# Kernel tuning notes

Measured on AMD Instinct MI355X. Metric: run time of the kernel, lower is better.

The kernel has to match this reference:

```python
import jax, jax.numpy as jnp
import numpy as np

DIV_COEF = 1.0
EPS = 1e-8  # torch.cosine_similarity default eps


def setup_inputs() -> dict:
    key = jax.random.key(0)
    id_ = jax.random.normal(key, (8192, 512), dtype=jnp.float32)
    return {"id": id_}


def reference(id):
    # cosine similarity via norm + GEMM (math identical to broadcast form)
    norms = jnp.linalg.norm(id, axis=1)                      # [N]
    dots = id @ id.T                                          # [N, N]
    sim = dots / jnp.maximum(norms[:, None] * norms[None, :], EPS)
    n = id.shape[0]
    # zero diagonal, clamp negatives to zero, mean over full NxN
    off_diag = 1.0 - jnp.eye(n, dtype=sim.dtype)
    id_sim = off_diag * sim
    l_id_div = jnp.mean(jnp.where(id_sim < 0, 0.0, id_sim))
    total_loss = DIV_COEF * l_id_div
    return (total_loss, l_id_div)
```

## Files before the change

### kernel.cpp

```cpp
#include <hip/hip_runtime.h>
#include <stdint.h>

#define NROWS 8192
#define KDIM  512
#define BM    128
#define BK    128
#define NKI   (KDIM / BK)
#define NT    (NROWS / BM)
#define NBLK  (NT * (NT + 1) / 2)

typedef __attribute__((ext_vector_type(4)))  int   i32x4;
typedef __attribute__((ext_vector_type(8)))  int   i32x8;
typedef __attribute__((ext_vector_type(16))) float f32x16;

#define SCALE1 0x7F7F7F7Fu

__device__ __forceinline__ void async_copy16(const unsigned char* g, unsigned char* l) {
  __builtin_amdgcn_global_load_lds(
      (const __attribute__((address_space(1))) unsigned int*)g,
      (__attribute__((address_space(3))) unsigned int*)l,
      16, 0, 0);
}

__global__ __launch_bounds__(256) void prep_kernel(
    const float* __restrict__ src, unsigned char* __restrict__ dst,
    float* __restrict__ acc) {
  const int row  = blockIdx.x * 4 + (threadIdx.x >> 6);
  const int lane = threadIdx.x & 63;
  const float4 v0 = ((const float4*)src)[row * 128 + lane * 2];
  const float4 v1 = ((const float4*)src)[row * 128 + lane * 2 + 1];
  float ss = v0.x * v0.x + v0.y * v0.y + v0.z * v0.z + v0.w * v0.w
           + v1.x * v1.x + v1.y * v1.y + v1.z * v1.z + v1.w * v1.w;
  #pragma unroll
  for (int off = 32; off > 0; off >>= 1) ss += __shfl_down(ss, off);
  const float rn = 1.0f / sqrtf(__shfl(ss, 0));
  if (row == 0 && lane == 0) *acc = 0.0f;
  int pk0 = __builtin_amdgcn_cvt_pk_fp8_f32(v0.x * rn, v0.y * rn, 0, false);
  pk0     = __builtin_amdgcn_cvt_pk_fp8_f32(v0.z * rn, v0.w * rn, pk0, true);
  int pk1 = __builtin_amdgcn_cvt_pk_fp8_f32(v1.x * rn, v1.y * rn, 0, false);
  pk1     = __builtin_amdgcn_cvt_pk_fp8_f32(v1.z * rn, v1.w * rn, pk1, true);
  const int cg  = lane >> 1;
  const int win = cg >> 3;
  const int p   = (cg & 7) ^ (row & 7);
  uint2 o; o.x = (unsigned int)pk0; o.y = (unsigned int)pk1;
  ((uint2*)dst)[row * 64 + win * 16 + p * 2 + (lane & 1)] = o;
}

__device__ __forceinline__ int tri_base(int b) {
  return b * NT - (b * (b - 1)) / 2;
}

__global__ __launch_bounds__(256) void sim_reduce_kernel(
    const unsigned char* __restrict__ idn, float* __restrict__ acc) {
  const int idx = blockIdx.x;
  const float Af = 2.0f * NT + 1.0f;
  int bi = (int)((Af - sqrtf(Af * Af - 8.0f * (float)idx)) * 0.5f);
  while (bi > 0 && tri_base(bi) > idx) bi--;
  while (tri_base(bi + 1) <= idx) bi++;
  const int bj = bi + (idx - tri_base(bi));

  __shared__ __align__(16) unsigned char As[2][BM * BK];
  __shared__ __align__(16) unsigned char Bs[2][BM * BK];

  const int tid  = threadIdx.x;
  const int lane = tid & 63;
  const int w    = tid >> 6;
  const int wr   = (w >> 1) * 64;
  const int wc   = (w & 1) * 64;
  const int l31  = lane & 31;
  const int kg   = lane >> 5;
  const int key  = lane & 7;

  f32x16 acc_f[2][2];
  #pragma unroll
  for (int i = 0; i < 2; i++)
    #pragma unroll
    for (int j = 0; j < 2; j++)
      #pragma unroll
      for (int k = 0; k < 16; k++) acc_f[i][j][k] = 0.f;

  const unsigned char* gA = idn + (size_t)(bi * BM + (tid >> 3)) * KDIM + (tid & 7) * 16;
  const unsigned char* gB = idn + (size_t)(bj * BM + (tid >> 3)) * KDIM + (tid & 7) * 16;
  const int ldso = tid * 16;

  #pragma unroll
  for (int i = 0; i < 4; i++) async_copy16(gA + (size_t)i * 16384, &As[0][ldso + i * 4096]);
  #pragma unroll
  for (int i = 0; i < 4; i++) async_copy16(gB + (size_t)i * 16384, &Bs[0][ldso + i * 4096]);

  #pragma unroll
  for (int t = 0; t < NKI; ++t) {
    const int cs = t & 1;
    if (t + 1 < NKI) {
      const int ns = cs ^ 1;
      const int ko = (t + 1) * BK;
      #pragma unroll
      for (int i = 0; i < 4; i++)
        async_copy16(gA + ko + (size_t)i * 16384, &As[ns][ldso + i * 4096]);
      #pragma unroll
      for (int i = 0; i < 4; i++)
        async_copy16(gB + ko + (size_t)i * 16384, &Bs[ns][ldso + i * 4096]);
      asm volatile("s_waitcnt vmcnt(8)" ::: "memory");
    } else {
      asm volatile("s_waitcnt vmcnt(0)" ::: "memory");
    }
    asm volatile("s_barrier" ::: "memory");

    #pragma unroll
    for (int s = 0; s < 2; s++) {
      const int c0 = s * 4 + kg * 2;
      const int pA0 = (c0 ^ key) * 16, pA1 = ((c0 + 1) ^ key) * 16;
      i32x8 a[2], b[2];
      #pragma unroll
      for (int r = 0; r < 2; r++) {
        const int rowA = (wr + r * 32 + l31) * BK;
        const int rowB = (wc + r * 32 + l31) * BK;
        i32x4 alo = *(const i32x4*)&As[cs][rowA + pA0];
        i32x4 ahi = *(const i32x4*)&As[cs][rowA + pA1];
        i32x4 blo = *(const i32x4*)&Bs[cs][rowB + pA0];
        i32x4 bhi = *(const i32x4*)&Bs[cs][rowB + pA1];
        a[r] = __builtin_shufflevector(alo, ahi, 0, 1, 2, 3, 4, 5, 6, 7);
        b[r] = __builtin_shufflevector(blo, bhi, 0, 1, 2, 3, 4, 5, 6, 7);
      }
      #pragma unroll
      for (int r = 0; r < 2; r++)
        #pragma unroll
        for (int c = 0; c < 2; c++)
          acc_f[r][c] = __builtin_amdgcn_mfma_scale_f32_32x32x64_f8f6f4(
              a[r], b[c], acc_f[r][c], 0, 0,
              0, SCALE1, 0, SCALE1);
    }

    asm volatile("s_barrier" ::: "memory");
  }

  float local = 0.f;
  const bool diag = (bi == bj);
  #pragma unroll
  for (int r = 0; r < 2; r++)
    #pragma unroll
    for (int c = 0; c < 2; c++)
      #pragma unroll
      for (int k = 0; k < 16; k++) {
        const int ri = wr + r * 32 + (k & 3) + 8 * (k >> 2) + 4 * kg;
        const int ci = wc + c * 32 + l31;
        float v = fmaxf(acc_f[r][c][k], 0.f);
        if (diag && ri == ci) v = 0.f;
        local += v;
      }

  #pragma unroll
  for (int off = 32; off > 0; off >>= 1) local += __shfl_down(local, off);
  __syncthreads();
  float* red = (float*)As;
  if (lane == 0) red[w] = local;
  __syncthreads();
  if (tid == 0) {
    float s = red[0] + red[1] + red[2] + red[3];
    if (!diag) s *= 2.f;
    atomicAdd(acc, s);
  }
}

__global__ void finalize_kernel(const float* __restrict__ acc, float* __restrict__ out) {
  const float m = *acc * (1.0f / ((float)NROWS * (float)NROWS));
  out[0] = m;
  out[1] = m;
}

extern "C" void kernel_launch(void* const* d_in, const int* in_sizes, int n_in,
                              void* d_out, int out_size, void* d_ws, size_t ws_size,
                              hipStream_t stream) {
  const float* id = (const float*)d_in[0];
  float* out = (float*)d_out;
  unsigned char* idn = (unsigned char*)d_ws;
  float* acc = (float*)((char*)d_ws + (size_t)NROWS * KDIM);

  prep_kernel<<<NROWS / 4, 256, 0, stream>>>(id, idn, acc);
  sim_reduce_kernel<<<NBLK, 256, 0, stream>>>(idn, acc);
  finalize_kernel<<<1, 1, 0, stream>>>(acc, out);
}
```

Baseline: 98.75 us.

## Keep A row-panel in registers and stream several B tiles per block

Each block now loads its full 128x512 FP8 A panel once into registers (via LDS) and loops over up to four B column tiles. B tiles are streamed in two K-halves through double-buffered LDS stages. This amortizes the A loads and cuts the block count, which should reduce global traffic, launch overhead and the triangular-index math. The cost is much higher register pressure (launch bounds with 2 blocks/CU), 64KB of LDS per block, and wasted blocks that exit early in the upper grid region.

```diff
diff --git a/kernel.cpp b/kernel.cpp
--- a/kernel.cpp
+++ b/kernel.cpp
@@ -3,11 +3,9 @@
 
 #define NROWS 8192
 #define KDIM  512
-#define BM    128
-#define BK    128
-#define NKI   (KDIM / BK)
-#define NT    (NROWS / BM)
-#define NBLK  (NT * (NT + 1) / 2)
+#define SR    128
+#define NT    (NROWS / SR)
+#define JCH   4
 
 typedef __attribute__((ext_vector_type(4)))  int   i32x4;
 typedef __attribute__((ext_vector_type(8)))  int   i32x8;
@@ -46,21 +44,17 @@
   ((uint2*)dst)[row * 64 + win * 16 + p * 2 + (lane & 1)] = o;
 }
 
-__device__ __forceinline__ int tri_base(int b) {
-  return b * NT - (b * (b - 1)) / 2;
-}
+__global__ __launch_bounds__(256, 2) void sim_reduce_kernel(
+    const unsigned char* __restrict__ idn, float* __restrict__ acc) {
+  const int bi = blockIdx.y;
+  const int jc = blockIdx.x;
+  if (jc * JCH + JCH <= bi) return;
+  const int j0 = (bi > jc * JCH) ? bi : jc * JCH;
+  const int j1 = jc * JCH + JCH;
 
-__global__ __launch_bounds__(256) void sim_reduce_kernel(
-    const unsigned char* __restrict__ idn, float* __restrict__ acc) {
-  const int idx = blockIdx.x;
-  const float Af = 2.0f * NT + 1.0f;
-  int bi = (int)((Af - sqrtf(Af * Af - 8.0f * (float)idx)) * 0.5f);
-  while (bi > 0 && tri_base(bi) > idx) bi--;
-  while (tri_base(bi + 1) <= idx) bi++;
-  const int bj = bi + (idx - tri_base(bi));
-
-  __shared__ __align__(16) unsigned char As[2][BM * BK];
-  __shared__ __align__(16) unsigned char Bs[2][BM * BK];
+  __shared__ __align__(16) unsigned char smem[65536];
+  unsigned char* st0 = smem;
+  unsigned char* st1 = smem + 32768;
 
   const int tid  = threadIdx.x;
   const int lane = tid & 63;
@@ -69,97 +63,113 @@
   const int wc   = (w & 1) * 64;
   const int l31  = lane & 31;
   const int kg   = lane >> 5;
-  const int key  = lane & 7;
 
-  f32x16 acc_f[2][2];
+  {
+    const unsigned char* gA = idn + (size_t)(bi * SR + (tid >> 5)) * KDIM + (tid & 31) * 16;
+    #pragma unroll
+    for (int i = 0; i < 16; i++)
+      async_copy16(gA + (size_t)i * 8 * KDIM, smem + tid * 16 + i * 4096);
+    asm volatile("s_waitcnt vmcnt(0)" ::: "memory");
+    __syncthreads();
+  }
+  i32x8 af[2][8];
+  #pragma unroll
+  for (int rt = 0; rt < 2; rt++) {
+    const int row = wr + rt * 32 + l31;
+    const int r7  = row & 7;
+    #pragma unroll
+    for (int s = 0; s < 8; s++) {
+      const int c0 = s * 4 + kg * 2;
+      const int ad = row * 512 + (c0 >> 3) * 128 + ((c0 & 7) ^ r7) * 16;
+      i32x4 lo = *(const i32x4*)&smem[ad];
+      i32x4 hi = *(const i32x4*)&smem[ad ^ 16];
+      af[rt][s] = __builtin_shufflevector(lo, hi, 0, 1, 2, 3, 4, 5, 6, 7);
+    }
+  }
+  asm volatile("s_waitcnt lgkmcnt(0)" ::: "memory");
+  __syncthreads();
+
+  f32x16 accf[2][2];
   #pragma unroll
   for (int i = 0; i < 2; i++)
     #pragma unroll
     for (int j = 0; j < 2; j++)
       #pragma unroll
-      for (int k = 0; k < 16; k++) acc_f[i][j][k] = 0.f;
+      for (int k = 0; k < 16; k++) accf[i][j][k] = 0.f;
+  float local = 0.f;
 
-  const unsigned char* gA = idn + (size_t)(bi * BM + (tid >> 3)) * KDIM + (tid & 7) * 16;
-  const unsigned char* gB = idn + (size_t)(bj * BM + (tid >> 3)) * KDIM + (tid & 7) * 16;
-  const int ldso = tid * 16;
-
-  #pragma unroll
-  for (int i = 0; i < 4; i++) async_copy16(gA + (size_t)i * 16384, &As[0][ldso + i * 4096]);
-  #pragma unroll
-  for (int i = 0; i < 4; i++) async_copy16(gB + (size_t)i * 16384, &Bs[0][ldso + i * 4096]);
-
-  #pragma unroll
-  for (int t = 0; t < NKI; ++t) {
-    const int cs = t & 1;
-    if (t + 1 < NKI) {
-      const int ns = cs ^ 1;
-      const int ko = (t + 1) * BK;
+  auto fillB = [&](int jj, int kh, unsigned char* stg) {
+    const unsigned char* gB =
+        idn + (size_t)(jj * SR + (tid >> 4)) * KDIM + kh * 256 + (tid & 15) * 16;
+    #pragma unroll
+    for (int i = 0; i < 8; i++)
+      async_copy16(gB + (size_t)i * 16 * KDIM, stg + tid * 16 + i * 4096);
+  };
+  auto computeB = [&](const unsigned char* stg, int base_s) {
+    #pragma unroll
+    for (int sl = 0; sl < 4; sl++) {
+      i32x8 b[2];
       #pragma unroll
-      for (int i = 0; i < 4; i++)
-        async_copy16(gA + ko + (size_t)i * 16384, &As[ns][ldso + i * 4096]);
-      #pragma unroll
-      for (int i = 0; i < 4; i++)
-        async_copy16(gB + ko + (size_t)i * 16384, &Bs[ns][ldso + i * 4096]);
-      asm volatile("s_waitcnt vmcnt(8)" ::: "memory");
-    } else {
-      asm volatile("s_waitcnt vmcnt(0)" ::: "memory");
-    }
-    asm volatile("s_barrier" ::: "memory");
-
-    #pragma unroll
-    for (int s = 0; s < 2; s++) {
-      const int c0 = s * 4 + kg * 2;
-      const int pA0 = (c0 ^ key) * 16, pA1 = ((c0 + 1) ^ key) * 16;
-      i32x8 a[2], b[2];
-      #pragma unroll
-      for (int r = 0; r < 2; r++) {
-        const int rowA = (wr + r * 32 + l31) * BK;
-        const int rowB = (wc + r * 32 + l31) * BK;
-        i32x4 alo = *(const i32x4*)&As[cs][rowA + pA0];
-        i32x4 ahi = *(const i32x4*)&As[cs][rowA + pA1];
-        i32x4 blo = *(const i32x4*)&Bs[cs][rowB + pA0];
-        i32x4 bhi = *(const i32x4*)&Bs[cs][rowB + pA1];
-        a[r] = __builtin_shufflevector(alo, ahi, 0, 1, 2, 3, 4, 5, 6, 7);
-        b[r] = __builtin_shufflevector(blo, bhi, 0, 1, 2, 3, 4, 5, 6, 7);
+      for (int cc = 0; cc < 2; cc++) {
+        const int brow = wc + cc * 32 + l31;
+        const int lc0  = sl * 4 + kg * 2;
+        const int ad   = brow * 256 + (lc0 >> 3) * 128 + ((lc0 & 7) ^ (brow & 7)) * 16;
+        i32x4 lo = *(const i32x4*)&stg[ad];
+        i32x4 hi = *(const i32x4*)&stg[ad ^ 16];
+        b[cc] = __builtin_shufflevector(lo, hi, 0, 1, 2, 3, 4, 5, 6, 7);
       }
       #pragma unroll
-      for (int r = 0; r < 2; r++)
+      for (int rt = 0; rt < 2; rt++)
         #pragma unroll
-        for (int c = 0; c < 2; c++)
-          acc_f[r][c] = __builtin_amdgcn_mfma_scale_f32_32x32x64_f8f6f4(
-              a[r], b[c], acc_f[r][c], 0, 0,
+        for (int cc = 0; cc < 2; cc++)
+          accf[rt][cc] = __builtin_amdgcn_mfma_scale_f32_32x32x64_f8f6f4(
+              af[rt][base_s + sl], b[cc], accf[rt][cc], 0, 0,
               0, SCALE1, 0, SCALE1);
     }
+  };
 
+  fillB(j0, 0, st0);
+  fillB(j0, 1, st1);
+
+  for (int jj = j0; jj < j1; ++jj) {
+    const bool more = (jj + 1 < j1);
+    asm volatile("s_waitcnt vmcnt(8)" ::: "memory");
     asm volatile("s_barrier" ::: "memory");
+    computeB(st0, 0);
+    asm volatile("s_barrier" ::: "memory");
+    if (more) fillB(jj + 1, 0, st0);
+    if (more) { asm volatile("s_waitcnt vmcnt(8)" ::: "memory"); }
+    else      { asm volatile("s_waitcnt vmcnt(0)" ::: "memory"); }
+    asm volatile("s_barrier" ::: "memory");
+    computeB(st1, 4);
+    asm volatile("s_barrier" ::: "memory");
+    if (more) fillB(jj + 1, 1, st1);
+
+    const bool diag = (jj == bi);
+    float gs = 0.f;
+    #pragma unroll
+    for (int rt = 0; rt < 2; rt++)
+      #pragma unroll
+      for (int cc = 0; cc < 2; cc++)
+        #pragma unroll
+        for (int k = 0; k < 16; k++) {
+          const int ri = wr + rt * 32 + (k & 3) + 8 * (k >> 2) + 4 * kg;
+          const int ci = wc + cc * 32 + l31;
+          float v = fmaxf(accf[rt][cc][k], 0.f);
+          if (diag && ri == ci) v = 0.f;
+          gs += v;
+          accf[rt][cc][k] = 0.f;
+        }
+    local += diag ? gs : 2.f * gs;
   }
-
-  float local = 0.f;
-  const bool diag = (bi == bj);
-  #pragma unroll
-  for (int r = 0; r < 2; r++)
-    #pragma unroll
-    for (int c = 0; c < 2; c++)
-      #pragma unroll
-      for (int k = 0; k < 16; k++) {
-        const int ri = wr + r * 32 + (k & 3) + 8 * (k >> 2) + 4 * kg;
-        const int ci = wc + c * 32 + l31;
-        float v = fmaxf(acc_f[r][c][k], 0.f);
-        if (diag && ri == ci) v = 0.f;
-        local += v;
-      }
 
   #pragma unroll
   for (int off = 32; off > 0; off >>= 1) local += __shfl_down(local, off);
   __syncthreads();
-  float* red = (float*)As;
+  float* red = (float*)smem;
   if (lane == 0) red[w] = local;
   __syncthreads();
-  if (tid == 0) {
-    float s = red[0] + red[1] + red[2] + red[3];
-    if (!diag) s *= 2.f;
-    atomicAdd(acc, s);
-  }
+  if (tid == 0) atomicAdd(acc, red[0] + red[1] + red[2] + red[3]);
 }
 
 __global__ void finalize_kernel(const float* __restrict__ acc, float* __restrict__ out) {
@@ -177,6 +187,7 @@
   float* acc = (float*)((char*)d_ws + (size_t)NROWS * KDIM);
 
   prep_kernel<<<NROWS / 4, 256, 0, stream>>>(id, idn, acc);
-  sim_reduce_kernel<<<NBLK, 256, 0, stream>>>(idn, acc);
+  dim3 grid(NT / JCH * JCH / JCH * 1 * 16 / 16 * 16, NT);
+  sim_reduce_kernel<<<dim3(16, NT), 256, 0, stream>>>(idn, acc);
   finalize_kernel<<<1, 1, 0, stream>>>(acc, out);
 }
```

Result: slower. 123.1 us (+24.7%).
